# Kernel tuning notes

Hardware: AMD Instinct MI355X
Metric: run time of the kernel (lower is better)

## Reference

```python
import jax, jax.numpy as jnp
import numpy as np

N, E, D_IN, D_OUT = 16384, 4096, 256, 256


def _leaky(v):
    return jnp.where(v > 0, v, 0.1 * v)


def setup_inputs() -> dict:
    key = jax.random.key(0)
    ks = jax.random.split(key, 8)
    x = jax.random.normal(ks[0], (N, D_IN), dtype=jnp.float32)
    # 0/1 incidence mask, float32 (as multiplied in the torch code)
    H_shape = jax.random.randint(ks[1], (N, E), 0, 2).astype(jnp.float32)
    w1 = jax.random.normal(ks[2], (D_IN, D_OUT), dtype=jnp.float32)
    w2 = jax.random.normal(ks[3], (D_OUT, D_OUT), dtype=jnp.float32)
    a1 = jax.random.normal(ks[4], (D_OUT, 1), dtype=jnp.float32)
    a21 = jax.random.normal(ks[5], (D_OUT, 1), dtype=jnp.float32)
    a22 = jax.random.normal(ks[6], (D_OUT, 1), dtype=jnp.float32)
    return {"x": x, "H_shape": H_shape, "w1": w1, "w2": w2,
            "a1": a1, "a21": a21, "a22": a22}


def reference(x, H_shape, w1, w2, a1, a21, a22):
    xw1 = x @ w1                                  # [N, D]
    # node->edge attention (masked softmax-like over nodes, axis -2)
    f = _leaky(xw1) @ a1                          # [N, 1]
    e = jnp.exp(jnp.tanh(f / 8) * 8) * H_shape    # [N, E]
    e = e / jnp.sum(e, axis=-2, keepdims=True)    # normalize over nodes
    # edge features
    f = _leaky(e.T @ xw1)                         # [E, D]
    # edge->node attention (masked normalize over edges, axis -1)
    b = (_leaky(f @ w2) @ a21).T + _leaky(xw1) @ a22  # [1,E] + [N,1] -> [N,E]
    b = jnp.exp(jnp.tanh(b / 8) * 8) * H_shape
    b = b / jnp.sum(b, axis=-1, keepdims=True)
    return _leaky(b @ f @ w2)                     # [N, D]
```

## Files before the change

kernel.cpp:

```cpp
#include <hip/hip_runtime.h>


typedef __attribute__((ext_vector_type(8))) short short8;
typedef __attribute__((ext_vector_type(4))) float f32x4;
typedef __attribute__((ext_vector_type(4))) int int4v;
typedef __attribute__((ext_vector_type(4))) unsigned int uint4v;

__device__ __forceinline__ float leakyf(float v) { return v > 0.f ? v : 0.1f * v; }
__device__ __forceinline__ float fastrcp(float x) { return __builtin_amdgcn_rcpf(x); }

__device__ __forceinline__ float satexpf(float t) {
    float u = fminf(fmaxf(t * 0.25f, -30.f), 30.f);
    float p = __expf(u);
    float th = (p - 1.f) * fastrcp(p + 1.f);
    return __expf(8.f * th);
}

__device__ __forceinline__ short f2b(float v) {
    unsigned int x = __float_as_uint(v);
    x += 0x7fffu + ((x >> 16) & 1u);
    return (short)(x >> 16);
}
__device__ __forceinline__ float b2f(short s) {
    return __uint_as_float(((unsigned int)(unsigned short)s) << 16);
}

__global__ __launch_bounds__(256) void transpose_split(
        const float* __restrict__ src, short* __restrict__ dh,
        short* __restrict__ dl, int R, int C) {
    __shared__ float Ts[64][65];
    const int t = threadIdx.x;
    const long r0 = (long)blockIdx.x * 64;
    const long c0 = (long)blockIdx.y * 64;
    {
        const int row = t >> 2, cc = (t & 3) * 16;
        const float* p = src + (r0 + row) * (long)C + c0 + cc;
#pragma unroll
        for (int i = 0; i < 4; ++i) {
            f32x4 v = *reinterpret_cast<const f32x4*>(p + i * 4);
#pragma unroll
            for (int k = 0; k < 4; ++k) Ts[row][cc + i * 4 + k] = v[k];
        }
    }
    __syncthreads();
    {
        const int cl = t >> 2, ch = (t & 3) * 16;
        short8 h0, h1, l0, l1;
#pragma unroll
        for (int i = 0; i < 8; ++i) {
            float v = Ts[ch + i][cl];
            short h = f2b(v);
            h0[i] = h; l0[i] = f2b(v - b2f(h));
        }
#pragma unroll
        for (int i = 0; i < 8; ++i) {
            float v = Ts[ch + 8 + i][cl];
            short h = f2b(v);
            h1[i] = h; l1[i] = f2b(v - b2f(h));
        }
        short* qh = dh + (c0 + cl) * (long)R + r0 + ch;
        short* ql = dl + (c0 + cl) * (long)R + r0 + ch;
        *reinterpret_cast<short8*>(qh) = h0;
        *reinterpret_cast<short8*>(qh + 8) = h1;
        *reinterpret_cast<short8*>(ql) = l0;
        *reinterpret_cast<short8*>(ql + 8) = l1;
    }
}

__global__ __launch_bounds__(256) void transposeH_pack(
        const float* __restrict__ H, char* __restrict__ HbT,
        unsigned int* __restrict__ Hbits) {
    __shared__ float Ts[64][65];
    const int t = threadIdx.x;
    const long r0 = (long)blockIdx.x * 64;
    const long c0 = (long)blockIdx.y * 64;
    {
        const int row = t >> 2, cc = (t & 3) * 16;
        const float* p = H + (r0 + row) * 4096L + c0 + cc;
#pragma unroll
        for (int i = 0; i < 4; ++i) {
            f32x4 v = *reinterpret_cast<const f32x4*>(p + i * 4);
#pragma unroll
            for (int k = 0; k < 4; ++k) Ts[row][cc + i * 4 + k] = v[k];
        }
    }
    __syncthreads();
    {
        const int cl = t >> 2, ch = (t & 3) * 16;
        uint4v pk;
#pragma unroll
        for (int wv = 0; wv < 4; ++wv) {
            unsigned int u = 0;
#pragma unroll
            for (int b = 0; b < 4; ++b)
                u |= (Ts[ch + wv * 4 + b][cl] != 0.f ? 1u : 0u) << (8 * b);
            pk[wv] = u;
        }
        *reinterpret_cast<uint4v*>(HbT + (c0 + cl) * 16384L + r0 + ch) = pk;
    }
    if (t < 128) {
        const int nl = t >> 1, w = t & 1;
        unsigned int u = 0;
#pragma unroll
        for (int b = 0; b < 32; ++b)
            u |= (Ts[nl][w * 32 + b] != 0.f ? 1u : 0u) << b;
        Hbits[(r0 + nl) * 128 + (c0 >> 5) + w] = u;
    }
}

__global__ __launch_bounds__(256) void gemm_xw1(
        const float* __restrict__ A, const short* __restrict__ Bh,
        const short* __restrict__ Bl, float* __restrict__ C) {
    __shared__ short Ash[128][72];
    __shared__ short Asl[128][72];
    __shared__ short Bsh[64][72];
    __shared__ short Bsl[64][72];
    const int t = threadIdx.x;
    const int wid = t >> 6, lane = t & 63;
    const int wm = wid & 1, wn = wid >> 1;
    const int quad = lane >> 4, l15 = lane & 15;
    const long m0 = (long)blockIdx.x * 128;
    const long n0 = (long)blockIdx.y * 64;
    f32x4 acc[4][2];
#pragma unroll
    for (int i = 0; i < 4; ++i)
#pragma unroll
        for (int j = 0; j < 2; ++j)
#pragma unroll
            for (int r = 0; r < 4; ++r) acc[i][j][r] = 0.f;

    for (int kb = 0; kb < 256; kb += 64) {
#pragma unroll
        for (int it = 0; it < 4; ++it) {
            const int cid = t + it * 256;
            const int row = cid >> 3, c8 = (cid & 7) * 8;
            const float* ap = A + (m0 + row) * 256 + kb + c8;
            f32x4 v0 = *reinterpret_cast<const f32x4*>(ap);
            f32x4 v1 = *reinterpret_cast<const f32x4*>(ap + 4);
            short8 hi, lo;
#pragma unroll
            for (int k = 0; k < 4; ++k) {
                short h0 = f2b(v0[k]); hi[k] = h0; lo[k] = f2b(v0[k] - b2f(h0));
                short h1 = f2b(v1[k]); hi[4 + k] = h1; lo[4 + k] = f2b(v1[k] - b2f(h1));
            }
            *reinterpret_cast<short8*>(&Ash[row][c8]) = hi;
            *reinterpret_cast<short8*>(&Asl[row][c8]) = lo;
        }
#pragma unroll
        for (int it = 0; it < 2; ++it) {
            const int cid = t + it * 256;
            const int row = cid >> 3, c8 = (cid & 7) * 8;
            *reinterpret_cast<short8*>(&Bsh[row][c8]) =
                *reinterpret_cast<const short8*>(Bh + (n0 + row) * 256 + kb + c8);
            *reinterpret_cast<short8*>(&Bsl[row][c8]) =
                *reinterpret_cast<const short8*>(Bl + (n0 + row) * 256 + kb + c8);
        }
        __syncthreads();
#pragma unroll
        for (int ks = 0; ks < 2; ++ks) {
            short8 ah[4], al[4], bh[2], bl[2];
#pragma unroll
            for (int i = 0; i < 4; ++i) {
                ah[i] = *reinterpret_cast<const short8*>(&Ash[wm * 64 + i * 16 + l15][ks * 32 + quad * 8]);
                al[i] = *reinterpret_cast<const short8*>(&Asl[wm * 64 + i * 16 + l15][ks * 32 + quad * 8]);
            }
#pragma unroll
            for (int j = 0; j < 2; ++j) {
                bh[j] = *reinterpret_cast<const short8*>(&Bsh[wn * 32 + j * 16 + l15][ks * 32 + quad * 8]);
                bl[j] = *reinterpret_cast<const short8*>(&Bsl[wn * 32 + j * 16 + l15][ks * 32 + quad * 8]);
            }
#pragma unroll
            for (int i = 0; i < 4; ++i)
#pragma unroll
                for (int j = 0; j < 2; ++j) {
                    acc[i][j] = __builtin_amdgcn_mfma_f32_16x16x32_bf16(ah[i], bh[j], acc[i][j], 0, 0, 0);
                    acc[i][j] = __builtin_amdgcn_mfma_f32_16x16x32_bf16(ah[i], bl[j], acc[i][j], 0, 0, 0);
                    acc[i][j] = __builtin_amdgcn_mfma_f32_16x16x32_bf16(al[i], bh[j], acc[i][j], 0, 0, 0);
                }
        }
        __syncthreads();
    }
#pragma unroll
    for (int i = 0; i < 4; ++i) {
        const long grow = m0 + wm * 64 + i * 16 + quad * 4;
#pragma unroll
        for (int j = 0; j < 2; ++j) {
            const long gcol = n0 + wn * 32 + j * 16 + l15;
#pragma unroll
            for (int r = 0; r < 4; ++r)
                C[(grow + r) * 256 + gcol] = acc[i][j][r];
        }
    }
}

__global__ __launch_bounds__(256) void node_stats1(
        const float* __restrict__ xw1, const float* __restrict__ a1,
        const float* __restrict__ a22, float* __restrict__ g_out,
        float* __restrict__ dn, unsigned int* __restrict__ ddmax) {
    __shared__ float Mx[4][260];
    const int t = threadIdx.x;
    const int n0 = blockIdx.x * 64;
    const int r = t >> 2, q = t & 3;
    const long n = n0 + r;
    const float* xp = xw1 + n * 256 + q * 64;
    float vals[64];
    float facc = 0.f, dacc = 0.f;
#pragma unroll
    for (int i = 0; i < 16; ++i) {
        f32x4 v  = *reinterpret_cast<const f32x4*>(xp + i * 4);
        f32x4 b1 = *reinterpret_cast<const f32x4*>(a1 + q * 64 + i * 4);
        f32x4 b2 = *reinterpret_cast<const f32x4*>(a22 + q * 64 + i * 4);
#pragma unroll
        for (int k = 0; k < 4; ++k) {
            float lv = leakyf(v[k]);
            facc += lv * b1[k];
            dacc += lv * b2[k];
            vals[i * 4 + k] = v[k];
        }
    }
    facc += __shfl_xor(facc, 1); facc += __shfl_xor(facc, 2);
    dacc += __shfl_xor(dacc, 1); dacc += __shfl_xor(dacc, 2);
    const float g = satexpf(facc);
    if (q == 0) { dn[n] = dacc; g_out[n] = g; }
    float lm[64];
#pragma unroll
    for (int i = 0; i < 64; ++i) lm[i] = fabsf(vals[i] * g);
#pragma unroll
    for (int m = 4; m < 64; m <<= 1)
#pragma unroll
        for (int i = 0; i < 64; ++i) lm[i] = fmaxf(lm[i], __shfl_xor(lm[i], m));
    float gm = g;
#pragma unroll
    for (int m = 1; m < 64; m <<= 1) gm = fmaxf(gm, __shfl_xor(gm, m));
    const int wv = t >> 6, lane = t & 63;
    if (lane < 4) {
#pragma unroll
        for (int i = 0; i < 64; ++i) Mx[wv][lane * 64 + i] = lm[i];
    }
    if (lane == 0) Mx[wv][256] = gm;
    __syncthreads();
    if (t < 256) {
        float m = fmaxf(fmaxf(Mx[0][t], Mx[1][t]), fmaxf(Mx[2][t], Mx[3][t]));
        atomicMax(&ddmax[t], __float_as_uint(m));
    }
    if (t == 0) {
        float m = fmaxf(fmaxf(Mx[0][256], Mx[1][256]), fmaxf(Mx[2][256], Mx[3][256]));
        atomicMax(&ddmax[256], __float_as_uint(m));
    }
}

__global__ __launch_bounds__(256) void quantize_y(
        const float* __restrict__ xw1, const float* __restrict__ g_in,
        const unsigned int* __restrict__ ddmax, char* __restrict__ yQ) {
    __shared__ unsigned int Qh[257][16];
    __shared__ unsigned int Ql[257][16];
    const int t = threadIdx.x;
    const int n0 = blockIdx.x * 64;
    const int dd0 = (t >> 4) * 16;
    const int w = t & 15;
    const int r4 = w * 4;
    float s[16];
#pragma unroll
    for (int i = 0; i < 16; ++i)
        s[i] = 32512.f / __uint_as_float(ddmax[dd0 + i]);
    const float sg = 32512.f / __uint_as_float(ddmax[256]);
    unsigned int bh[16], bl[16];
#pragma unroll
    for (int i = 0; i < 16; ++i) { bh[i] = 0u; bl[i] = 0u; }
    unsigned int gh = 0u, gl = 0u;
#pragma unroll
    for (int rr = 0; rr < 4; ++rr) {
        const long n = n0 + r4 + rr;
        const float gg = g_in[n];
        const float* xp = xw1 + n * 256 + dd0;
#pragma unroll
        for (int c = 0; c < 4; ++c) {
            f32x4 v = *reinterpret_cast<const f32x4*>(xp + c * 4);
#pragma unroll
            for (int k = 0; k < 4; ++k) {
                const int i = c * 4 + k;
                int qv = __float2int_rn(v[k] * gg * s[i]);
                qv = max(-32639, min(32639, qv));
                const int qh = (qv + 128) >> 8;
                const int ql = qv - (qh << 8);
                bh[i] |= ((unsigned int)(qh & 255)) << (8 * rr);
                bl[i] |= ((unsigned int)(ql & 255)) << (8 * rr);
            }
        }
        if (t < 16) {
            int qv = __float2int_rn(gg * sg);
            qv = max(-32639, min(32639, qv));
            const int qh = (qv + 128) >> 8;
            const int ql = qv - (qh << 8);
            gh |= ((unsigned int)(qh & 255)) << (8 * rr);
            gl |= ((unsigned int)(ql & 255)) << (8 * rr);
        }
    }
#pragma unroll
    for (int i = 0; i < 16; ++i) { Qh[dd0 + i][w] = bh[i]; Ql[dd0 + i][w] = bl[i]; }
    if (t < 16) { Qh[256][t] = gh; Ql[256][t] = gl; }
    __syncthreads();
#pragma unroll
    for (int it = 0; it < 2; ++it) {
        const int dd = it * 256 + t;
        if (dd < 288) {
#pragma unroll
            for (int s2 = 0; s2 < 4; ++s2) {
                uint4v vh, vl;
                if (dd < 257) {
                    vh = *reinterpret_cast<const uint4v*>(&Qh[dd][s2 * 4]);
                    vl = *reinterpret_cast<const uint4v*>(&Ql[dd][s2 * 4]);
                } else {
#pragma unroll
                    for (int k = 0; k < 4; ++k) { vh[k] = 0u; vl[k] = 0u; }
                }
                *reinterpret_cast<uint4v*>(yQ + (long)dd * 16384 + n0 + s2 * 16) = vh;
                *reinterpret_cast<uint4v*>(yQ + (long)(288 + dd) * 16384 + n0 + s2 * 16) = vl;
            }
        }
    }
}

__global__ __launch_bounds__(256) void gemm_c1_i8(
        const char* __restrict__ Ab, const char* __restrict__ Bb,
        int* __restrict__ Cp) {
    __shared__ char As[128][144];
    __shared__ char Bs[96][144];
    const int t = threadIdx.x;
    const int wid = t >> 6, lane = t & 63;
    const int wm = wid & 1, wn = wid >> 1;
    const int quad = lane >> 4, l15 = lane & 15;
    const long m0 = (long)blockIdx.x * 128;
    const long n0 = (long)blockIdx.y * 96;
    const long k0 = (long)blockIdx.z * 4096;
    int* Cz = Cp + (long)blockIdx.z * (4096L * 576);
    int4v acc[4][3];
#pragma unroll
    for (int i = 0; i < 4; ++i)
#pragma unroll
        for (int j = 0; j < 3; ++j)
#pragma unroll
            for (int r = 0; r < 4; ++r) acc[i][j][r] = 0;

    for (int kb = 0; kb < 4096; kb += 128) {
#pragma unroll
        for (int it = 0; it < 4; ++it) {
            const int cid = t + it * 256;
            const int row = cid >> 3, seg = (cid & 7) * 16;
            *reinterpret_cast<uint4v*>(&As[row][seg]) =
                *reinterpret_cast<const uint4v*>(Ab + (m0 + row) * 16384 + k0 + kb + seg);
        }
#pragma unroll
        for (int it = 0; it < 3; ++it) {
            const int cid = t + it * 256;
            const int row = cid >> 3, seg = (cid & 7) * 16;
            *reinterpret_cast<uint4v*>(&Bs[row][seg]) =
                *reinterpret_cast<const uint4v*>(Bb + (n0 + row) * 16384 + k0 + kb + seg);
        }
        __syncthreads();
#pragma unroll
        for (int ks = 0; ks < 2; ++ks) {
            int4v af[4], bf[3];
#pragma unroll
            for (int i = 0; i < 4; ++i)
                af[i] = *reinterpret_cast<const int4v*>(
                        &As[wm * 64 + i * 16 + l15][ks * 64 + quad * 16]);
#pragma unroll
            for (int j = 0; j < 3; ++j)
                bf[j] = *reinterpret_cast<const int4v*>(
                        &Bs[wn * 48 + j * 16 + l15][ks * 64 + quad * 16]);
#pragma unroll
            for (int i = 0; i < 4; ++i)
#pragma unroll
                for (int j = 0; j < 3; ++j)
                    acc[i][j] = __builtin_amdgcn_mfma_i32_16x16x64_i8(
                            af[i], bf[j], acc[i][j], 0, 0, 0);
        }
        __syncthreads();
    }
#pragma unroll
    for (int i = 0; i < 4; ++i) {
        const long grow = m0 + wm * 64 + i * 16 + quad * 4;
#pragma unroll
        for (int j = 0; j < 3; ++j) {
            const long gcol = n0 + wn * 48 + j * 16 + l15;
#pragma unroll
            for (int r = 0; r < 4; ++r)
                Cz[(grow + r) * 576 + gcol] = acc[i][j][r];
        }
    }
}

__global__ __launch_bounds__(256) void reduce_C1(
        const int* __restrict__ C1p, const unsigned int* __restrict__ ddmax,
        float* __restrict__ C1) {
    const int i = blockIdx.x * 256 + threadIdx.x;
    const int j = i / 288, dd = i - j * 288;
    const int* p = C1p + (long)j * 576 + dd;
    int sh = 0, sl = 0;
#pragma unroll
    for (int z = 0; z < 4; ++z) {
        const int* pz = p + (long)z * 4096 * 576;
        sh += pz[0]; sl += pz[288];
    }
    const float scale = __uint_as_float(ddmax[dd]) * (1.f / 32512.f);
    C1[i] = (float)(sh * 256 + sl) * scale;
}

__global__ __launch_bounds__(256) void gemm_G(
        const float* __restrict__ C1, const short* __restrict__ w2Th,
        const short* __restrict__ w2Tl, const float* __restrict__ a21,
        short* __restrict__ GT, float* __restrict__ cat) {
    __shared__ short Ash[64][72];
    __shared__ short Asl[64][72];
    __shared__ short Bsh[64][72];
    __shared__ short Bsl[64][72];
    __shared__ float Gs[64][65];
    const int t = threadIdx.x;
    const int wid = t >> 6, lane = t & 63;
    const int wm = wid & 1, wn = wid >> 1;
    const int quad = lane >> 4, l15 = lane & 15;
    const long j0 = (long)blockIdx.x * 64;
    const long d0 = (long)blockIdx.y * 64;
    f32x4 acc[2][2];
#pragma unroll
    for (int i = 0; i < 2; ++i)
#pragma unroll
        for (int j = 0; j < 2; ++j)
#pragma unroll
            for (int r = 0; r < 4; ++r) acc[i][j][r] = 0.f;

    for (int kb = 0; kb < 256; kb += 64) {
#pragma unroll
        for (int it = 0; it < 2; ++it) {
            const int cid = t + it * 256;
            const int row = cid >> 3, c8 = (cid & 7) * 8;
            const float rd = fastrcp(C1[(j0 + row) * 288 + 256]);
            const float* ap = C1 + (j0 + row) * 288 + kb + c8;
            f32x4 v0 = *reinterpret_cast<const f32x4*>(ap);
            f32x4 v1 = *reinterpret_cast<const f32x4*>(ap + 4);
            short8 hi, lo;
#pragma unroll
            for (int k = 0; k < 4; ++k) {
                float f0 = leakyf(v0[k] * rd);
                float f1 = leakyf(v1[k] * rd);
                short h0 = f2b(f0); hi[k] = h0; lo[k] = f2b(f0 - b2f(h0));
                short h1 = f2b(f1); hi[4 + k] = h1; lo[4 + k] = f2b(f1 - b2f(h1));
            }
            *reinterpret_cast<short8*>(&Ash[row][c8]) = hi;
            *reinterpret_cast<short8*>(&Asl[row][c8]) = lo;
            *reinterpret_cast<short8*>(&Bsh[row][c8]) =
                *reinterpret_cast<const short8*>(w2Th + (d0 + row) * 256 + kb + c8);
            *reinterpret_cast<short8*>(&Bsl[row][c8]) =
                *reinterpret_cast<const short8*>(w2Tl + (d0 + row) * 256 + kb + c8);
        }
        __syncthreads();
#pragma unroll
        for (int ks = 0; ks < 2; ++ks) {
            short8 ah[2], al[2], bh[2], bl[2];
#pragma unroll
            for (int i = 0; i < 2; ++i) {
                ah[i] = *reinterpret_cast<const short8*>(&Ash[wm * 32 + i * 16 + l15][ks * 32 + quad * 8]);
                al[i] = *reinterpret_cast<const short8*>(&Asl[wm * 32 + i * 16 + l15][ks * 32 + quad * 8]);
            }
#pragma unroll
            for (int j = 0; j < 2; ++j) {
                bh[j] = *reinterpret_cast<const short8*>(&Bsh[wn * 32 + j * 16 + l15][ks * 32 + quad * 8]);
                bl[j] = *reinterpret_cast<const short8*>(&Bsl[wn * 32 + j * 16 + l15][ks * 32 + quad * 8]);
            }
#pragma unroll
            for (int i = 0; i < 2; ++i)
#pragma unroll
                for (int j = 0; j < 2; ++j) {
                    acc[i][j] = __builtin_amdgcn_mfma_f32_16x16x32_bf16(ah[i], bh[j], acc[i][j], 0, 0, 0);
                    acc[i][j] = __builtin_amdgcn_mfma_f32_16x16x32_bf16(ah[i], bl[j], acc[i][j], 0, 0, 0);
                    acc[i][j] = __builtin_amdgcn_mfma_f32_16x16x32_bf16(al[i], bh[j], acc[i][j], 0, 0, 0);
                }
        }
        __syncthreads();
    }
#pragma unroll
    for (int i = 0; i < 2; ++i)
#pragma unroll
        for (int j = 0; j < 2; ++j)
#pragma unroll
            for (int r = 0; r < 4; ++r)
                Gs[wm * 32 + i * 16 + quad * 4 + r][wn * 32 + j * 16 + l15] = acc[i][j][r];
    __syncthreads();
    {
        const int jl = t >> 2, q = t & 3;
        float cp = 0.f;
#pragma unroll
        for (int i = 0; i < 16; ++i) {
            const int d = q * 16 + i;
            cp += leakyf(Gs[jl][d]) * a21[d0 + d];
        }
        cp += __shfl_xor(cp, 1); cp += __shfl_xor(cp, 2);
        if (q == 0) atomicAdd(&cat[j0 + jl], cp);
    }
    {
        const int dl = t >> 2, q = t & 3;
        short8 pk0, pk1;
#pragma unroll
        for (int i = 0; i < 8; ++i) pk0[i] = f2b(Gs[q * 16 + i][dl]);
#pragma unroll
        for (int i = 0; i < 8; ++i) pk1[i] = f2b(Gs[q * 16 + 8 + i][dl]);
        short* gp = GT + (d0 + dl) * 4096 + j0 + q * 16;
        *reinterpret_cast<short8*>(gp) = pk0;
        *reinterpret_cast<short8*>(gp + 8) = pk1;
    }
}

__global__ __launch_bounds__(256) void edge_weights(
        const unsigned int* __restrict__ Hbits, const float* __restrict__ cat,
        const float* __restrict__ dn, short* __restrict__ Bmat,
        float* __restrict__ rsum) {
    const long n = blockIdx.x;
    const int t = threadIdx.x;
    const float dv = dn[n];
    const unsigned int w = Hbits[n * 128 + (t >> 1)];
    const int bo = (t & 1) * 16;
    short* bp = Bmat + n * 4096 + t * 16;
    float acc = 0.f;
    short8 pk0, pk1;
#pragma unroll
    for (int c = 0; c < 4; ++c) {
        f32x4 cv = *reinterpret_cast<const f32x4*>(cat + t * 16 + c * 4);
#pragma unroll
        for (int k = 0; k < 4; ++k) {
            const int kk = c * 4 + k;
            const float s = ((w >> (bo + kk)) & 1u) ? satexpf(cv[k] + dv) : 0.f;
            const short sb = f2b(s);
            if (kk < 8) pk0[kk] = sb; else pk1[kk - 8] = sb;
            acc += b2f(sb);
        }
    }
    *reinterpret_cast<short8*>(bp) = pk0;
    *reinterpret_cast<short8*>(bp + 8) = pk1;
#pragma unroll
    for (int m = 1; m < 64; m <<= 1) acc += __shfl_xor(acc, m);
    __shared__ float wsum[4];
    if ((t & 63) == 0) wsum[t >> 6] = acc;
    __syncthreads();
    if (t == 0) rsum[n] = wsum[0] + wsum[1] + wsum[2] + wsum[3];
}

template<int BM, int BN>
__global__ __launch_bounds__(256) void gemm_final(
        const short* __restrict__ Ab, const short* __restrict__ Bb,
        float* __restrict__ C, const float* __restrict__ aux) {
    constexpr int BK = 64;
    constexpr int TM = BM / 32, TN = BN / 32;
    __shared__ short As[BM][BK + 8];
    __shared__ short Bs[BN][BK + 8];
    const int t = threadIdx.x;
    const int wid = t >> 6, lane = t & 63;
    const int wm = wid & 1, wn = wid >> 1;
    const int quad = lane >> 4, l15 = lane & 15;
    const long m0 = (long)blockIdx.x * BM;
    const long n0 = (long)blockIdx.y * BN;
    f32x4 acc[TM][TN];
#pragma unroll
    for (int i = 0; i < TM; ++i)
#pragma unroll
        for (int j = 0; j < TN; ++j)
#pragma unroll
            for (int r = 0; r < 4; ++r) acc[i][j][r] = 0.f;

    for (int kb = 0; kb < 4096; kb += BK) {
#pragma unroll
        for (int it = 0; it < BM * BK / 2048; ++it) {
            const int cid = t + it * 256;
            const int row = cid >> 3, c8 = (cid & 7) * 8;
            *reinterpret_cast<short8*>(&As[row][c8]) =
                *reinterpret_cast<const short8*>(Ab + (m0 + row) * 4096 + kb + c8);
        }
#pragma unroll
        for (int it = 0; it < BN * BK / 2048; ++it) {
            const int cid = t + it * 256;
            const int row = cid >> 3, c8 = (cid & 7) * 8;
            *reinterpret_cast<short8*>(&Bs[row][c8]) =
                *reinterpret_cast<const short8*>(Bb + (n0 + row) * 4096 + kb + c8);
        }
        __syncthreads();
#pragma unroll
        for (int ks = 0; ks < 2; ++ks) {
            short8 af[TM], bf[TN];
#pragma unroll
            for (int i = 0; i < TM; ++i)
                af[i] = *reinterpret_cast<const short8*>(
                        &As[wm * (BM / 2) + i * 16 + l15][ks * 32 + quad * 8]);
#pragma unroll
            for (int j = 0; j < TN; ++j)
                bf[j] = *reinterpret_cast<const short8*>(
                        &Bs[wn * (BN / 2) + j * 16 + l15][ks * 32 + quad * 8]);
#pragma unroll
            for (int i = 0; i < TM; ++i)
#pragma unroll
                for (int j = 0; j < TN; ++j)
                    acc[i][j] = __builtin_amdgcn_mfma_f32_16x16x32_bf16(
                            af[i], bf[j], acc[i][j], 0, 0, 0);
        }
        __syncthreads();
    }
#pragma unroll
    for (int i = 0; i < TM; ++i) {
        const long grow = m0 + wm * (BM / 2) + i * 16 + quad * 4;
#pragma unroll
        for (int j = 0; j < TN; ++j) {
            const long gcol = n0 + wn * (BN / 2) + j * 16 + l15;
#pragma unroll
            for (int r = 0; r < 4; ++r)
                C[(grow + r) * 256 + gcol] =
                    leakyf(acc[i][j][r] * fastrcp(aux[grow + r]));
        }
    }
}

extern "C" void kernel_launch(void* const* d_in, const int* in_sizes, int n_in,
                              void* d_out, int out_size, void* d_ws, size_t ws_size,
                              hipStream_t stream) {
    const float* x   = (const float*)d_in[0];
    const float* H   = (const float*)d_in[1];
    const float* w1  = (const float*)d_in[2];
    const float* w2  = (const float*)d_in[3];
    const float* a1  = (const float*)d_in[4];
    const float* a21 = (const float*)d_in[5];
    const float* a22 = (const float*)d_in[6];
    float* out = (float*)d_out;
    char* ws = (char*)d_ws;

    float* xw1   = (float*)(ws + 0);
    int*   C1p   = (int*)(ws + 0);
    short* Bmat  = (short*)(ws + 0);
    char*  HbT   = (char*)(ws + 67108864);
    char*  yQ    = (char*)(ws + 134217728);
    float* dn    = (float*)(ws + 143654912);
    float* g     = (float*)(ws + 143720448);
    unsigned int* ddmax = (unsigned int*)(ws + 143785984);
    short* w1Th  = (short*)(ws + 143790080);
    short* w1Tl  = (short*)(ws + 143921152);
    short* w2Th  = (short*)(ws + 144052224);
    short* w2Tl  = (short*)(ws + 144183296);
    float* C1    = (float*)(ws + 144314368);
    short* GT    = (short*)(ws + 149032960);
    float* cat   = (float*)(ws + 151130112);
    float* rsum  = (float*)(ws + 151146496);
    unsigned int* Hbits = (unsigned int*)(ws + 151212032);

    hipMemsetAsync(ddmax, 0, 288 * sizeof(unsigned int), stream);
    hipMemsetAsync(cat, 0, 4096 * sizeof(float), stream);

    transpose_split<<<dim3(4, 4), 256, 0, stream>>>(w1, w1Th, w1Tl, 256, 256);
    transpose_split<<<dim3(4, 4), 256, 0, stream>>>(w2, w2Th, w2Tl, 256, 256);
    transposeH_pack<<<dim3(256, 64), 256, 0, stream>>>(H, HbT, Hbits);

    gemm_xw1<<<dim3(128, 4), 256, 0, stream>>>(x, w1Th, w1Tl, xw1);
    node_stats1<<<dim3(256), 256, 0, stream>>>(xw1, a1, a22, g, dn, ddmax);
    quantize_y<<<dim3(256), 256, 0, stream>>>(xw1, g, ddmax, yQ);

    gemm_c1_i8<<<dim3(32, 6, 4), 256, 0, stream>>>(HbT, yQ, C1p);
    reduce_C1<<<dim3(4608), 256, 0, stream>>>(C1p, ddmax, C1);

    gemm_G<<<dim3(64, 4), 256, 0, stream>>>(C1, w2Th, w2Tl, a21, GT, cat);

    edge_weights<<<dim3(16384), 256, 0, stream>>>(Hbits, cat, dn, Bmat, rsum);

    gemm_final<64, 128><<<dim3(256, 2), 256, 0, stream>>>(Bmat, GT, out, rsum);
}
```

Measured before the change: 673.3 us.

## Fuse edge-weight generation into final GEMM and restructure int8 C1 GEMM split

Merges the edge_weights kernel into the final GEMM. Each block now computes its bf16 attention tile on the fly from the packed H bits and cat, plus the row sums, so the 128MB Bmat write and read-back go away. The int8 C1 GEMM now computes the hi and lo quantized halves in the same block, sharing the A tile loads, and splits K 8 ways with float partials. The two weight transposes are merged into one launch. The fused kernel uses only 256 blocks with heavy shared memory, and each block recomputes the exps while reloading all of GT for every K step.

```diff
diff --git a/kernel.cpp b/kernel.cpp
--- a/kernel.cpp
+++ b/kernel.cpp
@@ -25,16 +25,19 @@
     return __uint_as_float(((unsigned int)(unsigned short)s) << 16);
 }
 
-__global__ __launch_bounds__(256) void transpose_split(
-        const float* __restrict__ src, short* __restrict__ dh,
-        short* __restrict__ dl, int R, int C) {
+__global__ __launch_bounds__(256) void transpose_split2(
+        const float* __restrict__ s0, short* __restrict__ dh0, short* __restrict__ dl0,
+        const float* __restrict__ s1, short* __restrict__ dh1, short* __restrict__ dl1) {
+    const float* src = blockIdx.z ? s1 : s0;
+    short* dh = blockIdx.z ? dh1 : dh0;
+    short* dl = blockIdx.z ? dl1 : dl0;
     __shared__ float Ts[64][65];
     const int t = threadIdx.x;
     const long r0 = (long)blockIdx.x * 64;
     const long c0 = (long)blockIdx.y * 64;
     {
         const int row = t >> 2, cc = (t & 3) * 16;
-        const float* p = src + (r0 + row) * (long)C + c0 + cc;
+        const float* p = src + (r0 + row) * 256 + c0 + cc;
 #pragma unroll
         for (int i = 0; i < 4; ++i) {
             f32x4 v = *reinterpret_cast<const f32x4*>(p + i * 4);
@@ -58,8 +61,8 @@
             short h = f2b(v);
             h1[i] = h; l1[i] = f2b(v - b2f(h));
         }
-        short* qh = dh + (c0 + cl) * (long)R + r0 + ch;
-        short* ql = dl + (c0 + cl) * (long)R + r0 + ch;
+        short* qh = dh + (c0 + cl) * 256 + r0 + ch;
+        short* ql = dl + (c0 + cl) * 256 + r0 + ch;
         *reinterpret_cast<short8*>(qh) = h0;
         *reinterpret_cast<short8*>(qh + 8) = h1;
         *reinterpret_cast<short8*>(ql) = l0;
@@ -323,26 +326,27 @@
 
 __global__ __launch_bounds__(256) void gemm_c1_i8(
         const char* __restrict__ Ab, const char* __restrict__ Bb,
-        int* __restrict__ Cp) {
+        float* __restrict__ Cp) {
     __shared__ char As[128][144];
-    __shared__ char Bs[96][144];
+    __shared__ char Bsh[96][144];
+    __shared__ char Bsl[96][144];
     const int t = threadIdx.x;
     const int wid = t >> 6, lane = t & 63;
     const int wm = wid & 1, wn = wid >> 1;
     const int quad = lane >> 4, l15 = lane & 15;
     const long m0 = (long)blockIdx.x * 128;
     const long n0 = (long)blockIdx.y * 96;
-    const long k0 = (long)blockIdx.z * 4096;
-    int* Cz = Cp + (long)blockIdx.z * (4096L * 576);
-    int4v acc[4][3];
+    const long k0 = (long)blockIdx.z * 2048;
+    float* Cz = Cp + (long)blockIdx.z * (4096L * 288);
+    int4v acch[4][3], accl[4][3];
 #pragma unroll
     for (int i = 0; i < 4; ++i)
 #pragma unroll
         for (int j = 0; j < 3; ++j)
 #pragma unroll
-            for (int r = 0; r < 4; ++r) acc[i][j][r] = 0;
-
-    for (int kb = 0; kb < 4096; kb += 128) {
+            for (int r = 0; r < 4; ++r) { acch[i][j][r] = 0; accl[i][j][r] = 0; }
+
+    for (int kb = 0; kb < 2048; kb += 128) {
 #pragma unroll
         for (int it = 0; it < 4; ++it) {
             const int cid = t + it * 256;
@@ -354,27 +358,33 @@
         for (int it = 0; it < 3; ++it) {
             const int cid = t + it * 256;
             const int row = cid >> 3, seg = (cid & 7) * 16;
-            *reinterpret_cast<uint4v*>(&Bs[row][seg]) =
+            *reinterpret_cast<uint4v*>(&Bsh[row][seg]) =
                 *reinterpret_cast<const uint4v*>(Bb + (n0 + row) * 16384 + k0 + kb + seg);
+            *reinterpret_cast<uint4v*>(&Bsl[row][seg]) =
+                *reinterpret_cast<const uint4v*>(Bb + (288 + n0 + row) * 16384 + k0 + kb + seg);
         }
         __syncthreads();
 #pragma unroll
         for (int ks = 0; ks < 2; ++ks) {
-            int4v af[4], bf[3];
+            int4v af[4], bh[3], bl[3];
 #pragma unroll
             for (int i = 0; i < 4; ++i)
                 af[i] = *reinterpret_cast<const int4v*>(
                         &As[wm * 64 + i * 16 + l15][ks * 64 + quad * 16]);
 #pragma unroll
-            for (int j = 0; j < 3; ++j)
-                bf[j] = *reinterpret_cast<const int4v*>(
-                        &Bs[wn * 48 + j * 16 + l15][ks * 64 + quad * 16]);
+            for (int j = 0; j < 3; ++j) {
+                bh[j] = *reinterpret_cast<const int4v*>(
+                        &Bsh[wn * 48 + j * 16 + l15][ks * 64 + quad * 16]);
+                bl[j] = *reinterpret_cast<const int4v*>(
+                        &Bsl[wn * 48 + j * 16 + l15][ks * 64 + quad * 16]);
+            }
 #pragma unroll
             for (int i = 0; i < 4; ++i)
 #pragma unroll
-                for (int j = 0; j < 3; ++j)
-                    acc[i][j] = __builtin_amdgcn_mfma_i32_16x16x64_i8(
-                            af[i], bf[j], acc[i][j], 0, 0, 0);
+                for (int j = 0; j < 3; ++j) {
+                    acch[i][j] = __builtin_amdgcn_mfma_i32_16x16x64_i8(af[i], bh[j], acch[i][j], 0, 0, 0);
+                    accl[i][j] = __builtin_amdgcn_mfma_i32_16x16x64_i8(af[i], bl[j], accl[i][j], 0, 0, 0);
+                }
         }
         __syncthreads();
     }
@@ -386,25 +396,21 @@
             const long gcol = n0 + wn * 48 + j * 16 + l15;
 #pragma unroll
             for (int r = 0; r < 4; ++r)
-                Cz[(grow + r) * 576 + gcol] = acc[i][j][r];
+                Cz[(grow + r) * 288 + gcol] =
+                    256.f * (float)acch[i][j][r] + (float)accl[i][j][r];
         }
     }
 }
 
 __global__ __launch_bounds__(256) void reduce_C1(
-        const int* __restrict__ C1p, const unsigned int* __restrict__ ddmax,
+        const float* __restrict__ C1p, const unsigned int* __restrict__ ddmax,
         float* __restrict__ C1) {
     const int i = blockIdx.x * 256 + threadIdx.x;
-    const int j = i / 288, dd = i - j * 288;
-    const int* p = C1p + (long)j * 576 + dd;
-    int sh = 0, sl = 0;
-#pragma unroll
-    for (int z = 0; z < 4; ++z) {
-        const int* pz = p + (long)z * 4096 * 576;
-        sh += pz[0]; sl += pz[288];
-    }
-    const float scale = __uint_as_float(ddmax[dd]) * (1.f / 32512.f);
-    C1[i] = (float)(sh * 256 + sl) * scale;
+    const int dd = i % 288;
+    float s = 0.f;
+#pragma unroll
+    for (int z = 0; z < 8; ++z) s += C1p[(long)z * 4096 * 288 + i];
+    C1[i] = s * (__uint_as_float(ddmax[dd]) * (1.f / 32512.f));
 }
 
 __global__ __launch_bounds__(256) void gemm_G(
@@ -511,108 +517,110 @@
     }
 }
 
-__global__ __launch_bounds__(256) void edge_weights(
+__global__ __launch_bounds__(256) void fused_out(
         const unsigned int* __restrict__ Hbits, const float* __restrict__ cat,
-        const float* __restrict__ dn, short* __restrict__ Bmat,
-        float* __restrict__ rsum) {
-    const long n = blockIdx.x;
-    const int t = threadIdx.x;
-    const float dv = dn[n];
-    const unsigned int w = Hbits[n * 128 + (t >> 1)];
-    const int bo = (t & 1) * 16;
-    short* bp = Bmat + n * 4096 + t * 16;
-    float acc = 0.f;
-    short8 pk0, pk1;
-#pragma unroll
-    for (int c = 0; c < 4; ++c) {
-        f32x4 cv = *reinterpret_cast<const f32x4*>(cat + t * 16 + c * 4);
-#pragma unroll
-        for (int k = 0; k < 4; ++k) {
-            const int kk = c * 4 + k;
-            const float s = ((w >> (bo + kk)) & 1u) ? satexpf(cv[k] + dv) : 0.f;
-            const short sb = f2b(s);
-            if (kk < 8) pk0[kk] = sb; else pk1[kk - 8] = sb;
-            acc += b2f(sb);
-        }
-    }
-    *reinterpret_cast<short8*>(bp) = pk0;
-    *reinterpret_cast<short8*>(bp + 8) = pk1;
-#pragma unroll
-    for (int m = 1; m < 64; m <<= 1) acc += __shfl_xor(acc, m);
-    __shared__ float wsum[4];
-    if ((t & 63) == 0) wsum[t >> 6] = acc;
-    __syncthreads();
-    if (t == 0) rsum[n] = wsum[0] + wsum[1] + wsum[2] + wsum[3];
-}
-
-template<int BM, int BN>
-__global__ __launch_bounds__(256) void gemm_final(
-        const short* __restrict__ Ab, const short* __restrict__ Bb,
-        float* __restrict__ C, const float* __restrict__ aux) {
-    constexpr int BK = 64;
-    constexpr int TM = BM / 32, TN = BN / 32;
-    __shared__ short As[BM][BK + 8];
-    __shared__ short Bs[BN][BK + 8];
+        const float* __restrict__ dn, const short* __restrict__ GT,
+        float* __restrict__ out) {
+    __shared__ float catS[4096];
+    __shared__ unsigned int bitsS[64][132];
+    __shared__ short As[64][72];
+    __shared__ short Bs[256][72];
+    __shared__ float rsS[64][4];
+    __shared__ float rinvS[64];
     const int t = threadIdx.x;
     const int wid = t >> 6, lane = t & 63;
     const int wm = wid & 1, wn = wid >> 1;
     const int quad = lane >> 4, l15 = lane & 15;
-    const long m0 = (long)blockIdx.x * BM;
-    const long n0 = (long)blockIdx.y * BN;
-    f32x4 acc[TM][TN];
-#pragma unroll
-    for (int i = 0; i < TM; ++i)
-#pragma unroll
-        for (int j = 0; j < TN; ++j)
-#pragma unroll
-            for (int r = 0; r < 4; ++r) acc[i][j][r] = 0.f;
-
-    for (int kb = 0; kb < 4096; kb += BK) {
-#pragma unroll
-        for (int it = 0; it < BM * BK / 2048; ++it) {
-            const int cid = t + it * 256;
-            const int row = cid >> 3, c8 = (cid & 7) * 8;
-            *reinterpret_cast<short8*>(&As[row][c8]) =
-                *reinterpret_cast<const short8*>(Ab + (m0 + row) * 4096 + kb + c8);
-        }
-#pragma unroll
-        for (int it = 0; it < BN * BK / 2048; ++it) {
+    const long m0 = (long)blockIdx.x * 64;
+    const int r = t & 63, jc = t >> 6;
+    const float drow = dn[m0 + r];
+
+#pragma unroll
+    for (int i = 0; i < 4; ++i) {
+        f32x4 v = *reinterpret_cast<const f32x4*>(cat + t * 16 + i * 4);
+        *reinterpret_cast<f32x4*>(&catS[t * 16 + i * 4]) = v;
+    }
+#pragma unroll
+    for (int it = 0; it < 8; ++it) {
+        const int cid = t + it * 256;
+        const int row = cid >> 5, ch = (cid & 31) * 4;
+        *reinterpret_cast<uint4v*>(&bitsS[row][ch]) =
+            *reinterpret_cast<const uint4v*>(Hbits + (m0 + row) * 128 + ch);
+    }
+
+    f32x4 acc[2][8];
+#pragma unroll
+    for (int i = 0; i < 2; ++i)
+#pragma unroll
+        for (int j = 0; j < 8; ++j)
+#pragma unroll
+            for (int x = 0; x < 4; ++x) acc[i][j][x] = 0.f;
+    float racc = 0.f;
+    __syncthreads();
+
+    for (int kb = 0; kb < 4096; kb += 64) {
+#pragma unroll
+        for (int it = 0; it < 8; ++it) {
             const int cid = t + it * 256;
             const int row = cid >> 3, c8 = (cid & 7) * 8;
             *reinterpret_cast<short8*>(&Bs[row][c8]) =
-                *reinterpret_cast<const short8*>(Bb + (n0 + row) * 4096 + kb + c8);
+                *reinterpret_cast<const short8*>(GT + row * 4096 + kb + c8);
+        }
+        {
+            const unsigned int w = bitsS[r][(kb >> 5) + (jc >> 1)];
+            const int bo = (jc & 1) * 16;
+            short8 pk0, pk1;
+#pragma unroll
+            for (int c = 0; c < 4; ++c) {
+                f32x4 cv = *reinterpret_cast<const f32x4*>(&catS[kb + jc * 16 + c * 4]);
+#pragma unroll
+                for (int k = 0; k < 4; ++k) {
+                    const int kk = c * 4 + k;
+                    const float s = ((w >> (bo + kk)) & 1u) ? satexpf(cv[k] + drow) : 0.f;
+                    const short sb = f2b(s);
+                    if (kk < 8) pk0[kk] = sb; else pk1[kk - 8] = sb;
+                    racc += b2f(sb);
+                }
+            }
+            *reinterpret_cast<short8*>(&As[r][jc * 16]) = pk0;
+            *reinterpret_cast<short8*>(&As[r][jc * 16 + 8]) = pk1;
         }
         __syncthreads();
 #pragma unroll
         for (int ks = 0; ks < 2; ++ks) {
-            short8 af[TM], bf[TN];
-#pragma unroll
-            for (int i = 0; i < TM; ++i)
+            short8 af[2], bf[8];
+#pragma unroll
+            for (int i = 0; i < 2; ++i)
                 af[i] = *reinterpret_cast<const short8*>(
-                        &As[wm * (BM / 2) + i * 16 + l15][ks * 32 + quad * 8]);
-#pragma unroll
-            for (int j = 0; j < TN; ++j)
+                        &As[wm * 32 + i * 16 + l15][ks * 32 + quad * 8]);
+#pragma unroll
+            for (int j = 0; j < 8; ++j)
                 bf[j] = *reinterpret_cast<const short8*>(
-                        &Bs[wn * (BN / 2) + j * 16 + l15][ks * 32 + quad * 8]);
-#pragma unroll
-            for (int i = 0; i < TM; ++i)
-#pragma unroll
-                for (int j = 0; j < TN; ++j)
+                        &Bs[wn * 128 + j * 16 + l15][ks * 32 + quad * 8]);
+#pragma unroll
+            for (int i = 0; i < 2; ++i)
+#pragma unroll
+                for (int j = 0; j < 8; ++j)
                     acc[i][j] = __builtin_amdgcn_mfma_f32_16x16x32_bf16(
                             af[i], bf[j], acc[i][j], 0, 0, 0);
         }
         __syncthreads();
     }
-#pragma unroll
-    for (int i = 0; i < TM; ++i) {
-        const long grow = m0 + wm * (BM / 2) + i * 16 + quad * 4;
-#pragma unroll
-        for (int j = 0; j < TN; ++j) {
-            const long gcol = n0 + wn * (BN / 2) + j * 16 + l15;
-#pragma unroll
-            for (int r = 0; r < 4; ++r)
-                C[(grow + r) * 256 + gcol] =
-                    leakyf(acc[i][j][r] * fastrcp(aux[grow + r]));
+    rsS[r][jc] = racc;
+    __syncthreads();
+    if (t < 64)
+        rinvS[t] = fastrcp(rsS[t][0] + rsS[t][1] + rsS[t][2] + rsS[t][3]);
+    __syncthreads();
+#pragma unroll
+    for (int i = 0; i < 2; ++i) {
+#pragma unroll
+        for (int j = 0; j < 8; ++j) {
+            const long gcol = wn * 128 + j * 16 + l15;
+#pragma unroll
+            for (int x = 0; x < 4; ++x) {
+                const int rl = wm * 32 + i * 16 + quad * 4 + x;
+                out[(m0 + rl) * 256 + gcol] = leakyf(acc[i][j][x] * rinvS[rl]);
+            }
         }
     }
 }
@@ -631,8 +639,7 @@
     char* ws = (char*)d_ws;
 
     float* xw1   = (float*)(ws + 0);
-    int*   C1p   = (int*)(ws + 0);
-    short* Bmat  = (short*)(ws + 0);
+    float* C1p   = (float*)(ws + 0);
     char*  HbT   = (char*)(ws + 67108864);
     char*  yQ    = (char*)(ws + 134217728);
     float* dn    = (float*)(ws + 143654912);
@@ -645,26 +652,23 @@
     float* C1    = (float*)(ws + 144314368);
     short* GT    = (short*)(ws + 149032960);
     float* cat   = (float*)(ws + 151130112);
-    float* rsum  = (float*)(ws + 151146496);
     unsigned int* Hbits = (unsigned int*)(ws + 151212032);
 
     hipMemsetAsync(ddmax, 0, 288 * sizeof(unsigned int), stream);
     hipMemsetAsync(cat, 0, 4096 * sizeof(float), stream);
 
-    transpose_split<<<dim3(4, 4), 256, 0, stream>>>(w1, w1Th, w1Tl, 256, 256);
-    transpose_split<<<dim3(4, 4), 256, 0, stream>>>(w2, w2Th, w2Tl, 256, 256);
+    transpose_split2<<<dim3(4, 4, 2), 256, 0, stream>>>(
+            w1, w1Th, w1Tl, w2, w2Th, w2Tl);
     transposeH_pack<<<dim3(256, 64), 256, 0, stream>>>(H, HbT, Hbits);
 
     gemm_xw1<<<dim3(128, 4), 256, 0, stream>>>(x, w1Th, w1Tl, xw1);
     node_stats1<<<dim3(256), 256, 0, stream>>>(xw1, a1, a22, g, dn, ddmax);
     quantize_y<<<dim3(256), 256, 0, stream>>>(xw1, g, ddmax, yQ);
 
-    gemm_c1_i8<<<dim3(32, 6, 4), 256, 0, stream>>>(HbT, yQ, C1p);
+    gemm_c1_i8<<<dim3(32, 3, 8), 256, 0, stream>>>(HbT, yQ, C1p);
     reduce_C1<<<dim3(4608), 256, 0, stream>>>(C1p, ddmax, C1);
 
     gemm_G<<<dim3(64, 4), 256, 0, stream>>>(C1, w2Th, w2Tl, a21, GT, cat);
 
-    edge_weights<<<dim3(16384), 256, 0, stream>>>(Hbits, cat, dn, Bmat, rsum);
-
-    gemm_final<64, 128><<<dim3(256, 2), 256, 0, stream>>>(Bmat, GT, out, rsum);
-}
+    fused_out<<<dim3(256), 256, 0, stream>>>(Hbits, cat, dn, GT, out);
+}
```

Result: no change. 682.5 us (+1.4%).
